# Optimization experiments

Measured on AMD Instinct MI355X. Metric: run time of the kernel, lower is better.

The kernel has to match this reference:

```python
import math
import jax, jax.numpy as jnp
import numpy as np

B, A, U, S, E, HYP, H = 16384, 32, 64, 2048, 32, 64, 4
ATTEND_REG_COEF = 1e-3


def setup_inputs() -> dict:
    key = jax.random.key(0)
    ks = jax.random.split(key, 12)
    sc = 0.05
    return {
        "agent_qs": jax.random.normal(ks[0], (B, A), jnp.float32),
        "states": jax.random.normal(ks[1], (B, S), jnp.float32),
        # per-head selector hypernet: Linear(S,HYP)+ReLU+Linear(HYP,E,no bias)
        "sel_w1": jax.random.normal(ks[2], (H, S, HYP), jnp.float32) * sc,
        "sel_b1": jax.random.normal(ks[3], (H, HYP), jnp.float32) * sc,
        "sel_w2": jax.random.normal(ks[4], (H, HYP, E), jnp.float32) * sc,
        # per-head key extractor: Linear(U,E,no bias)
        "key_w": jax.random.normal(ks[5], (H, U, E), jnp.float32) * sc,
        # V net: Linear(S,E)+ReLU+Linear(E,1)
        "v_w1": jax.random.normal(ks[6], (S, E), jnp.float32) * sc,
        "v_b1": jax.random.normal(ks[7], (E,), jnp.float32) * sc,
        "v_w2": jax.random.normal(ks[8], (E, 1), jnp.float32) * sc,
        "v_b2": jax.random.normal(ks[9], (1,), jnp.float32) * sc,
    }


def reference(agent_qs, states, sel_w1, sel_b1, sel_w2, key_w, v_w1, v_b1, v_w2, v_b2):
    # nonlinear=False, weighted_head=False, state_bias=True (defaults used here)
    unit_states = states[:, : A * U].reshape(-1, A, U)  # [B, A, U]

    # per-head selectors: [B, H, E]
    h1 = jax.nn.relu(jnp.einsum("bs,hsk->bhk", states, sel_w1) + sel_b1[None])
    selectors = jnp.einsum("bhk,hke->bhe", h1, sel_w2)

    # per-head, per-agent keys: [B, H, A, E]
    keys = jnp.einsum("bau,hue->bhae", unit_states, key_w)

    # attention logits [B, H, A] (matches selector @ stacked-keys in torch)
    logits = jnp.einsum("bhe,bhae->bha", selectors, keys)
    weights = jax.nn.softmax(logits / math.sqrt(E), axis=-1)  # [B, H, A]

    head_attend = jnp.sum(weights, axis=1)  # [B, A]

    v = jax.nn.relu(states @ v_w1 + v_b1) @ v_w2 + v_b2  # [B, 1]

    # coef * sum over heads of mean(logits_h ** 2)
    attend_mag_regs = ATTEND_REG_COEF * jnp.sum(jnp.mean(logits ** 2, axis=(0, 2)))

    # per-head entropy: -(p * log(p + 1e-8)).sum(agents).mean(batch) -> [H]
    head_entropies = -jnp.mean(
        jnp.sum(weights * jnp.log(weights + 1e-8), axis=-1), axis=0
    )

    return head_attend, v, attend_mag_regs, head_entropies
```

## Files before the change

kernel.cpp:

```cpp
#include <hip/hip_runtime.h>
#include <hip/hip_bf16.h>

#define B_N 16384
#define A_N 32
#define U_N 64
#define S_N 2048
#define E_N 32
#define HYP_N 64
#define H_N 4
#define NREAL 288
#define NPADG 320

#define WS_WT    0
#define WS_C1    1310720
#define WS_MB    (WS_C1 + 9437184)
#define WS_PMAG  (WS_MB + 32768)
#define WS_PENT  (WS_PMAG + 65536)

#define OUT_V   (B_N * A_N)
#define OUT_MAG (OUT_V + B_N)
#define OUT_ENT (OUT_MAG + 1)

typedef __attribute__((ext_vector_type(8))) short bf16x8_t;
typedef __attribute__((ext_vector_type(4))) float floatx4_t;

#define AS1(p) ((const __attribute__((address_space(1))) void*)(p))
#define AS3(p) ((__attribute__((address_space(3))) void*)(p))

__device__ __forceinline__ unsigned short f2b(float f) {
    union { float f; unsigned u; } v; v.f = f;
    unsigned r = v.u + 0x7FFFu + ((v.u >> 16) & 1u);
    return (unsigned short)(r >> 16);
}
__device__ __forceinline__ float b2f(unsigned x) {
    union { unsigned u; float f; } v; v.u = x << 16; return v.f;
}

__global__ __launch_bounds__(256) void pack_w_kernel(
        const float* __restrict__ sel_w1, const float* __restrict__ v_w1,
        const float* __restrict__ sel_w2, const float* __restrict__ key_w,
        unsigned short* __restrict__ Wt, unsigned short* __restrict__ Mb) {
    int idx = blockIdx.x * 256 + threadIdx.x;
    if (idx < NPADG * S_N) {
        int n = idx >> 11;
        int k = idx & 2047;
        float val = 0.0f;
        if (n < 256) {
            int h = n >> 6, kk = n & 63;
            val = sel_w1[((size_t)h * S_N + k) * HYP_N + kk];
        } else if (n < NREAL) {
            val = v_w1[(size_t)k * E_N + (n - 256)];
        }
        Wt[idx] = f2b(val);
    } else if (idx < NPADG * S_N + H_N * U_N * HYP_N) {
        int j = idx - NPADG * S_N;
        int h = j >> 12, u = (j >> 6) & 63, k = j & 63;
        const float* kw = key_w + ((size_t)h * U_N + u) * E_N;
        const float* w2 = sel_w2 + ((size_t)h * HYP_N + k) * E_N;
        float s = 0.0f;
#pragma unroll
        for (int e = 0; e < E_N; ++e) s = fmaf(kw[e], w2[e], s);
        Mb[j] = f2b(s);
    }
}

#define GM_BM 64
#define GM_BK 64

__global__ __launch_bounds__(512) void gemm3_kernel(
        const float* __restrict__ states, const unsigned short* __restrict__ Wt,
        const float* __restrict__ sel_b1, const float* __restrict__ v_b1,
        unsigned short* __restrict__ C1) {
    __shared__ __align__(16) unsigned short Asm[GM_BM * GM_BK];
    __shared__ __align__(16) unsigned short Bsm[NPADG * GM_BK];

    const int t = threadIdx.x;
    const int lane = t & 63;
    const int w = t >> 6;
    const int m0 = blockIdx.x * GM_BM;
    const int mw = (w & 1) * 32;
    const int nw = (w >> 1) * 80;

    const int ar = t >> 3, acl = t & 7;
    const float* ap = states + (size_t)(m0 + ar) * S_N + acl * 8;

    floatx4_t acc[2][5] = {};

    float4 a0 = *(const float4*)(ap);
    float4 a1 = *(const float4*)(ap + 4);
    {
        int ph = acl ^ (ar & 7);
        uint4 o;
        o.x = (unsigned)f2b(a0.x) | ((unsigned)f2b(a0.y) << 16);
        o.y = (unsigned)f2b(a0.z) | ((unsigned)f2b(a0.w) << 16);
        o.z = (unsigned)f2b(a1.x) | ((unsigned)f2b(a1.y) << 16);
        o.w = (unsigned)f2b(a1.z) | ((unsigned)f2b(a1.w) << 16);
        *(uint4*)(Asm + (size_t)(ar * 8 + ph) * 8) = o;
    }
#pragma unroll
    for (int i = 0; i < 5; ++i) {
        int p = i * 512 + t, n = p >> 3, sl = p & 7;
        int cl = sl ^ (n & 7);
        __builtin_amdgcn_global_load_lds(AS1(Wt + (size_t)n * S_N + cl * 8),
                                         AS3(Bsm + p * 8), 16, 0, 0);
    }
    __syncthreads();

    for (int it = 0; it < 32; ++it) {
        if (it < 31) {
            const float* g = ap + (it + 1) * GM_BK;
            a0 = *(const float4*)(g);
            a1 = *(const float4*)(g + 4);
        }
#pragma unroll
        for (int s = 0; s < 2; ++s) {
            const int c = s * 4 + (lane >> 4);
            bf16x8_t afr[2];
#pragma unroll
            for (int mt = 0; mt < 2; ++mt) {
                int r = mw + mt * 16 + (lane & 15);
                int ph = c ^ (r & 7);
                afr[mt] = *(const bf16x8_t*)(Asm + r * 64 + ph * 8);
            }
#pragma unroll
            for (int nt = 0; nt < 5; ++nt) {
                int n = nw + nt * 16 + (lane & 15);
                int ph = c ^ (n & 7);
                bf16x8_t bfr = *(const bf16x8_t*)(Bsm + n * 64 + ph * 8);
                acc[0][nt] = __builtin_amdgcn_mfma_f32_16x16x32_bf16(
                    afr[0], bfr, acc[0][nt], 0, 0, 0);
                acc[1][nt] = __builtin_amdgcn_mfma_f32_16x16x32_bf16(
                    afr[1], bfr, acc[1][nt], 0, 0, 0);
            }
        }
        __syncthreads();
        if (it < 31) {
            int k0 = (it + 1) * GM_BK;
            {
                int ph = acl ^ (ar & 7);
                uint4 o;
                o.x = (unsigned)f2b(a0.x) | ((unsigned)f2b(a0.y) << 16);
                o.y = (unsigned)f2b(a0.z) | ((unsigned)f2b(a0.w) << 16);
                o.z = (unsigned)f2b(a1.x) | ((unsigned)f2b(a1.y) << 16);
                o.w = (unsigned)f2b(a1.z) | ((unsigned)f2b(a1.w) << 16);
                *(uint4*)(Asm + (size_t)(ar * 8 + ph) * 8) = o;
            }
#pragma unroll
            for (int i = 0; i < 5; ++i) {
                int p = i * 512 + t, n = p >> 3, sl = p & 7;
                int cl = sl ^ (n & 7);
                __builtin_amdgcn_global_load_lds(
                    AS1(Wt + (size_t)n * S_N + k0 + cl * 8),
                    AS3(Bsm + p * 8), 16, 0, 0);
            }
            __syncthreads();
        }
    }

#pragma unroll
    for (int nt = 0; nt < 5; ++nt) {
        int n = nw + nt * 16 + (lane & 15);
        if (n >= NREAL) continue;
        float bias = (n < 256) ? sel_b1[n] : v_b1[n - 256];
#pragma unroll
        for (int mt = 0; mt < 2; ++mt) {
            int rbase = m0 + mw + mt * 16 + (lane >> 4) * 4;
#pragma unroll
            for (int rg = 0; rg < 4; ++rg) {
                float v = acc[mt][nt][rg] + bias;
                C1[(size_t)(rbase + rg) * NREAL + n] = f2b(v > 0.0f ? v : 0.0f);
            }
        }
    }
}

#define EP_ROWS 32
#define H1_STRIDE 312
#define TS_STRIDE 260

__global__ __launch_bounds__(256) void epilogue3_kernel(
        const float* __restrict__ states, const unsigned short* __restrict__ C1,
        const unsigned short* __restrict__ Mb,
        const float* __restrict__ v_w2, const float* __restrict__ v_b2,
        float* __restrict__ out, float* __restrict__ pmag, float* __restrict__ pent) {
    __shared__ __align__(16) unsigned short h1s[EP_ROWS][H1_STRIDE];
    __shared__ float ts[EP_ROWS][TS_STRIDE];

    const int t = threadIdx.x;
    const int w = t >> 6;
    const int lane = t & 63;
    const int b0 = blockIdx.x * EP_ROWS;

#pragma unroll
    for (int i = 0; i < 5; ++i) {
        int c = i * 256 + t;
        if (c < EP_ROWS * 36) {
            int r = c / 36, cc = c - r * 36;
            int n = cc * 8;
            uint4 v = *(const uint4*)(C1 + (size_t)(b0 + r) * NREAL + n);
            int idx = (n < 256) ? ((n >> 6) * 72 + (n & 63))
                                : (((n - 256) >> 3) * 72 + 64);
            *(uint4*)&h1s[r][idx] = v;
        }
    }
    __syncthreads();

    {
        const int h = w;
        floatx4_t tacc[2][4] = {};
#pragma unroll
        for (int s = 0; s < 2; ++s) {
            int k0 = s * 32 + (lane >> 4) * 8;
            bf16x8_t bfr[4];
#pragma unroll
            for (int ut = 0; ut < 4; ++ut) {
                int u = ut * 16 + (lane & 15);
                bfr[ut] = *(const bf16x8_t*)(Mb + ((size_t)(h * U_N + u) * 64) + k0);
            }
#pragma unroll
            for (int mt = 0; mt < 2; ++mt) {
                int r = mt * 16 + (lane & 15);
                bf16x8_t afr = *(const bf16x8_t*)&h1s[r][h * 72 + k0];
#pragma unroll
                for (int ut = 0; ut < 4; ++ut)
                    tacc[mt][ut] = __builtin_amdgcn_mfma_f32_16x16x32_bf16(
                        afr, bfr[ut], tacc[mt][ut], 0, 0, 0);
            }
        }
#pragma unroll
        for (int mt = 0; mt < 2; ++mt)
#pragma unroll
            for (int ut = 0; ut < 4; ++ut)
#pragma unroll
                for (int rg = 0; rg < 4; ++rg) {
                    int r = mt * 16 + (lane >> 4) * 4 + rg;
                    int u = ut * 16 + (lane & 15);
                    ts[r][h * U_N + u] = tacc[mt][ut][rg];
                }
    }
    __syncthreads();

    const int a = lane & 31, uh = lane >> 5;
    float4 cur[8], nxt[8];
    {
        const float* up = states + (size_t)(b0 + w * 8) * S_N + a * 64 + uh * 32;
#pragma unroll
        for (int i = 0; i < 8; ++i) cur[i] = ((const float4*)up)[i];
    }
    for (int rr = 0; rr < 8; ++rr) {
        int r = w * 8 + rr;
        int b = b0 + r;
        if (rr < 7) {
            const float* up = states + (size_t)(b + 1) * S_N + a * 64 + uh * 32;
#pragma unroll
            for (int i = 0; i < 8; ++i) nxt[i] = ((const float4*)up)[i];
        }
        float pl[4];
#pragma unroll
        for (int h = 0; h < 4; ++h) {
            const float* tp = &ts[r][h * U_N + uh * 32];
            float s = 0.0f;
#pragma unroll
            for (int i = 0; i < 8; ++i) {
                float4 t4 = *(const float4*)(tp + i * 4);
                s = fmaf(cur[i].x, t4.x, s);
                s = fmaf(cur[i].y, t4.y, s);
                s = fmaf(cur[i].z, t4.z, s);
                s = fmaf(cur[i].w, t4.w, s);
            }
            pl[h] = s + __shfl_xor(s, 32, 64);
        }
        float mg = pl[0]*pl[0] + pl[1]*pl[1] + pl[2]*pl[2] + pl[3]*pl[3];
#pragma unroll
        for (int o = 16; o > 0; o >>= 1) mg += __shfl_xor(mg, o, 32);
        float hatt = 0.0f;
        float entv[4];
#pragma unroll
        for (int h = 0; h < 4; ++h) {
            float x = pl[h] * 0.17677669529663687f;
            float m = x;
#pragma unroll
            for (int o = 16; o > 0; o >>= 1) m = fmaxf(m, __shfl_xor(m, o, 32));
            float p = expf(x - m);
            float den = p;
#pragma unroll
            for (int o = 16; o > 0; o >>= 1) den += __shfl_xor(den, o, 32);
            float wv = p / den;
            hatt += wv;
            float e = wv * logf(wv + 1e-8f);
#pragma unroll
            for (int o = 16; o > 0; o >>= 1) e += __shfl_xor(e, o, 32);
            entv[h] = e;
        }
        if (uh == 0) {
            out[(size_t)b * A_N + a] = hatt;
            float pv = b2f((unsigned)h1s[r][(a >> 3) * 72 + 64 + (a & 7)]) * v_w2[a];
#pragma unroll
            for (int o = 16; o > 0; o >>= 1) pv += __shfl_xor(pv, o, 32);
            if (a == 0) {
                out[OUT_V + b] = pv + v_b2[0];
                pmag[b] = mg;
#pragma unroll
                for (int h = 0; h < 4; ++h) pent[(size_t)h * B_N + b] = entv[h];
            }
        }
#pragma unroll
        for (int i = 0; i < 8; ++i) cur[i] = nxt[i];
    }
}

__global__ __launch_bounds__(256) void finalize_kernel(
        const float* __restrict__ pmag, const float* __restrict__ pent,
        float* __restrict__ out) {
    int which = blockIdx.x;
    const float* src = (which == 0) ? pmag : (pent + (size_t)(which - 1) * B_N);
    float s = 0.0f;
    for (int i = threadIdx.x; i < B_N; i += 256) s += src[i];
#pragma unroll
    for (int o = 32; o > 0; o >>= 1) s += __shfl_xor(s, o, 64);
    __shared__ float red[4];
    if ((threadIdx.x & 63) == 0) red[threadIdx.x >> 6] = s;
    __syncthreads();
    if (threadIdx.x == 0) {
        float tot = red[0] + red[1] + red[2] + red[3];
        if (which == 0) out[OUT_MAG] = 1e-3f * tot / (float)(B_N * A_N);
        else out[OUT_ENT + which - 1] = -tot / (float)B_N;
    }
}

extern "C" void kernel_launch(void* const* d_in, const int* in_sizes, int n_in,
                              void* d_out, int out_size, void* d_ws, size_t ws_size,
                              hipStream_t stream) {
    const float* states = (const float*)d_in[1];
    const float* sel_w1 = (const float*)d_in[2];
    const float* sel_b1 = (const float*)d_in[3];
    const float* sel_w2 = (const float*)d_in[4];
    const float* key_w  = (const float*)d_in[5];
    const float* v_w1   = (const float*)d_in[6];
    const float* v_b1   = (const float*)d_in[7];
    const float* v_w2   = (const float*)d_in[8];
    const float* v_b2   = (const float*)d_in[9];
    float* out = (float*)d_out;
    char* wsb  = (char*)d_ws;

    unsigned short* Wt  = (unsigned short*)(wsb + WS_WT);
    unsigned short* C1  = (unsigned short*)(wsb + WS_C1);
    unsigned short* Mb  = (unsigned short*)(wsb + WS_MB);
    float* pmag         = (float*)(wsb + WS_PMAG);
    float* pent         = (float*)(wsb + WS_PENT);

    pack_w_kernel<<<dim3((NPADG * S_N + H_N * U_N * HYP_N + 255) / 256),
                    dim3(256), 0, stream>>>(sel_w1, v_w1, sel_w2, key_w, Wt, Mb);
    gemm3_kernel<<<dim3(B_N / GM_BM), dim3(512), 0, stream>>>(
        states, Wt, sel_b1, v_b1, C1);
    epilogue3_kernel<<<dim3(B_N / EP_ROWS), dim3(256), 0, stream>>>(
        states, C1, Mb, v_w2, v_b2, out, pmag, pent);
    finalize_kernel<<<dim3(5), dim3(256), 0, stream>>>(pmag, pent, out);
}
```

Measured before the change: 295.7 us.

## Fuse hypernet GEMM and attention epilogue into one kernel via shared memory

Merges the GEMM kernel and the epilogue kernel into one kernel that keeps the ReLU'd hidden activations in LDS rather than writing them to a bf16 global buffer and reading them back. The row tile shrinks from 64 to 32 rows with 256 threads, and the B-tile and score buffers share an aliased LDS pool. This removes one launch and the round trip through the intermediate C1 buffer. In exchange, each block reloads the full weight tile for half as many rows, which doubles weight traffic per output row and may lower MFMA efficiency.

```diff
diff --git a/kernel.cpp b/kernel.cpp
--- a/kernel.cpp
+++ b/kernel.cpp
@@ -12,8 +12,7 @@
 #define NPADG 320
 
 #define WS_WT    0
-#define WS_C1    1310720
-#define WS_MB    (WS_C1 + 9437184)
+#define WS_MB    1310720
 #define WS_PMAG  (WS_MB + 32768)
 #define WS_PENT  (WS_PMAG + 65536)
 
@@ -64,22 +63,28 @@
     }
 }
 
-#define GM_BM 64
-#define GM_BK 64
-
-__global__ __launch_bounds__(512) void gemm3_kernel(
+#define FM_BM 32
+#define FM_BK 64
+#define H1_STRIDE 312
+#define TS_STRIDE 260
+
+__global__ __launch_bounds__(256) void fused_kernel(
         const float* __restrict__ states, const unsigned short* __restrict__ Wt,
         const float* __restrict__ sel_b1, const float* __restrict__ v_b1,
-        unsigned short* __restrict__ C1) {
-    __shared__ __align__(16) unsigned short Asm[GM_BM * GM_BK];
-    __shared__ __align__(16) unsigned short Bsm[NPADG * GM_BK];
+        const unsigned short* __restrict__ Mb,
+        const float* __restrict__ v_w2, const float* __restrict__ v_b2,
+        float* __restrict__ out, float* __restrict__ pmag, float* __restrict__ pent) {
+    __shared__ __align__(16) char pool[4096 + 40960 + H1_STRIDE * FM_BM * 2];
+    unsigned short* Asm = (unsigned short*)pool;
+    unsigned short* Bsm = (unsigned short*)(pool + 4096);
+    float*          tsb = (float*)(pool + 4096);
+    unsigned short* h1b = (unsigned short*)(pool + 4096 + 40960);
 
     const int t = threadIdx.x;
     const int lane = t & 63;
     const int w = t >> 6;
-    const int m0 = blockIdx.x * GM_BM;
-    const int mw = (w & 1) * 32;
-    const int nw = (w >> 1) * 80;
+    const int m0 = blockIdx.x * FM_BM;
+    const int nw = w * 80;
 
     const int ar = t >> 3, acl = t & 7;
     const float* ap = states + (size_t)(m0 + ar) * S_N + acl * 8;
@@ -98,8 +103,8 @@
         *(uint4*)(Asm + (size_t)(ar * 8 + ph) * 8) = o;
     }
 #pragma unroll
-    for (int i = 0; i < 5; ++i) {
-        int p = i * 512 + t, n = p >> 3, sl = p & 7;
+    for (int i = 0; i < 10; ++i) {
+        int p = i * 256 + t, n = p >> 3, sl = p & 7;
         int cl = sl ^ (n & 7);
         __builtin_amdgcn_global_load_lds(AS1(Wt + (size_t)n * S_N + cl * 8),
                                          AS3(Bsm + p * 8), 16, 0, 0);
@@ -108,7 +113,7 @@
 
     for (int it = 0; it < 32; ++it) {
         if (it < 31) {
-            const float* g = ap + (it + 1) * GM_BK;
+            const float* g = ap + (it + 1) * FM_BK;
             a0 = *(const float4*)(g);
             a1 = *(const float4*)(g + 4);
         }
@@ -118,7 +123,7 @@
             bf16x8_t afr[2];
 #pragma unroll
             for (int mt = 0; mt < 2; ++mt) {
-                int r = mw + mt * 16 + (lane & 15);
+                int r = mt * 16 + (lane & 15);
                 int ph = c ^ (r & 7);
                 afr[mt] = *(const bf16x8_t*)(Asm + r * 64 + ph * 8);
             }
@@ -135,7 +140,7 @@
         }
         __syncthreads();
         if (it < 31) {
-            int k0 = (it + 1) * GM_BK;
+            int k0 = (it + 1) * FM_BK;
             {
                 int ph = acl ^ (ar & 7);
                 uint4 o;
@@ -146,8 +151,8 @@
                 *(uint4*)(Asm + (size_t)(ar * 8 + ph) * 8) = o;
             }
 #pragma unroll
-            for (int i = 0; i < 5; ++i) {
-                int p = i * 512 + t, n = p >> 3, sl = p & 7;
+            for (int i = 0; i < 10; ++i) {
+                int p = i * 256 + t, n = p >> 3, sl = p & 7;
                 int cl = sl ^ (n & 7);
                 __builtin_amdgcn_global_load_lds(
                     AS1(Wt + (size_t)n * S_N + k0 + cl * 8),
@@ -162,45 +167,16 @@
         int n = nw + nt * 16 + (lane & 15);
         if (n >= NREAL) continue;
         float bias = (n < 256) ? sel_b1[n] : v_b1[n - 256];
+        int slot = (n < 256) ? ((n >> 6) * 72 + (n & 63))
+                             : (((n - 256) >> 3) * 72 + 64 + ((n - 256) & 7));
 #pragma unroll
         for (int mt = 0; mt < 2; ++mt) {
-            int rbase = m0 + mw + mt * 16 + (lane >> 4) * 4;
 #pragma unroll
             for (int rg = 0; rg < 4; ++rg) {
+                int r = mt * 16 + (lane >> 4) * 4 + rg;
                 float v = acc[mt][nt][rg] + bias;
-                C1[(size_t)(rbase + rg) * NREAL + n] = f2b(v > 0.0f ? v : 0.0f);
-            }
-        }
-    }
-}
-
-#define EP_ROWS 32
-#define H1_STRIDE 312
-#define TS_STRIDE 260
-
-__global__ __launch_bounds__(256) void epilogue3_kernel(
-        const float* __restrict__ states, const unsigned short* __restrict__ C1,
-        const unsigned short* __restrict__ Mb,
-        const float* __restrict__ v_w2, const float* __restrict__ v_b2,
-        float* __restrict__ out, float* __restrict__ pmag, float* __restrict__ pent) {
-    __shared__ __align__(16) unsigned short h1s[EP_ROWS][H1_STRIDE];
-    __shared__ float ts[EP_ROWS][TS_STRIDE];
-
-    const int t = threadIdx.x;
-    const int w = t >> 6;
-    const int lane = t & 63;
-    const int b0 = blockIdx.x * EP_ROWS;
-
-#pragma unroll
-    for (int i = 0; i < 5; ++i) {
-        int c = i * 256 + t;
-        if (c < EP_ROWS * 36) {
-            int r = c / 36, cc = c - r * 36;
-            int n = cc * 8;
-            uint4 v = *(const uint4*)(C1 + (size_t)(b0 + r) * NREAL + n);
-            int idx = (n < 256) ? ((n >> 6) * 72 + (n & 63))
-                                : (((n - 256) >> 3) * 72 + 64);
-            *(uint4*)&h1s[r][idx] = v;
+                h1b[r * H1_STRIDE + slot] = f2b(v > 0.0f ? v : 0.0f);
+            }
         }
     }
     __syncthreads();
@@ -220,7 +196,7 @@
 #pragma unroll
             for (int mt = 0; mt < 2; ++mt) {
                 int r = mt * 16 + (lane & 15);
-                bf16x8_t afr = *(const bf16x8_t*)&h1s[r][h * 72 + k0];
+                bf16x8_t afr = *(const bf16x8_t*)(h1b + r * H1_STRIDE + h * 72 + k0);
 #pragma unroll
                 for (int ut = 0; ut < 4; ++ut)
                     tacc[mt][ut] = __builtin_amdgcn_mfma_f32_16x16x32_bf16(
@@ -235,7 +211,7 @@
                 for (int rg = 0; rg < 4; ++rg) {
                     int r = mt * 16 + (lane >> 4) * 4 + rg;
                     int u = ut * 16 + (lane & 15);
-                    ts[r][h * U_N + u] = tacc[mt][ut][rg];
+                    tsb[r * TS_STRIDE + h * U_N + u] = tacc[mt][ut][rg];
                 }
     }
     __syncthreads();
@@ -243,13 +219,13 @@
     const int a = lane & 31, uh = lane >> 5;
     float4 cur[8], nxt[8];
     {
-        const float* up = states + (size_t)(b0 + w * 8) * S_N + a * 64 + uh * 32;
+        const float* up = states + (size_t)(m0 + w * 8) * S_N + a * 64 + uh * 32;
 #pragma unroll
         for (int i = 0; i < 8; ++i) cur[i] = ((const float4*)up)[i];
     }
     for (int rr = 0; rr < 8; ++rr) {
         int r = w * 8 + rr;
-        int b = b0 + r;
+        int b = m0 + r;
         if (rr < 7) {
             const float* up = states + (size_t)(b + 1) * S_N + a * 64 + uh * 32;
 #pragma unroll
@@ -258,7 +234,7 @@
         float pl[4];
 #pragma unroll
         for (int h = 0; h < 4; ++h) {
-            const float* tp = &ts[r][h * U_N + uh * 32];
+            const float* tp = &tsb[r * TS_STRIDE + h * U_N + uh * 32];
             float s = 0.0f;
 #pragma unroll
             for (int i = 0; i < 8; ++i) {
@@ -294,7 +270,8 @@
         }
         if (uh == 0) {
             out[(size_t)b * A_N + a] = hatt;
-            float pv = b2f((unsigned)h1s[r][(a >> 3) * 72 + 64 + (a & 7)]) * v_w2[a];
+            float pv = b2f((unsigned)h1b[r * H1_STRIDE + (a >> 3) * 72 + 64 + (a & 7)])
+                       * v_w2[a];
 #pragma unroll
             for (int o = 16; o > 0; o >>= 1) pv += __shfl_xor(pv, o, 32);
             if (a == 0) {
@@ -344,16 +321,13 @@
     char* wsb  = (char*)d_ws;
 
     unsigned short* Wt  = (unsigned short*)(wsb + WS_WT);
-    unsigned short* C1  = (unsigned short*)(wsb + WS_C1);
     unsigned short* Mb  = (unsigned short*)(wsb + WS_MB);
     float* pmag         = (float*)(wsb + WS_PMAG);
     float* pent         = (float*)(wsb + WS_PENT);
 
     pack_w_kernel<<<dim3((NPADG * S_N + H_N * U_N * HYP_N + 255) / 256),
                     dim3(256), 0, stream>>>(sel_w1, v_w1, sel_w2, key_w, Wt, Mb);
-    gemm3_kernel<<<dim3(B_N / GM_BM), dim3(512), 0, stream>>>(
-        states, Wt, sel_b1, v_b1, C1);
-    epilogue3_kernel<<<dim3(B_N / EP_ROWS), dim3(256), 0, stream>>>(
-        states, C1, Mb, v_w2, v_b2, out, pmag, pent);
+    fused_kernel<<<dim3(B_N / FM_BM), dim3(256), 0, stream>>>(
+        states, Wt, sel_b1, v_b1, Mb, v_w2, v_b2, out, pmag, pent);
     finalize_kernel<<<dim3(5), dim3(256), 0, stream>>>(pmag, pent, out);
 }
```

Result: faster. 286.2 us (-3.2%).
